# Performance work log

Measured on AMD Instinct MI355X. Metric: run time of the kernel, lower is better.

## Reference

```python
import jax, jax.numpy as jnp
import numpy as np

N = 100000      # nodes
E = 1600000     # edges (avg degree 16)
IN, HID, OUT = 128, 128, 64


def setup_inputs() -> dict:
    key = jax.random.key(0)
    k1, k2, k3, k4 = jax.random.split(key, 4)
    x = jax.random.normal(k1, (N, IN), dtype=jnp.float32)
    edge_index = jax.random.randint(k2, (2, E), 0, N, dtype=jnp.int64)
    # GCNConv linear weights (glorot-ish scale) and zero biases
    W1 = jax.random.normal(k3, (IN, HID), dtype=jnp.float32) * (1.0 / np.sqrt(IN))
    b1 = jnp.zeros((HID,), jnp.float32)
    W2 = jax.random.normal(k4, (HID, OUT), dtype=jnp.float32) * (1.0 / np.sqrt(HID))
    b2 = jnp.zeros((OUT,), jnp.float32)
    return {"x": x, "edge_index": edge_index, "W1": W1, "b1": b1, "W2": W2, "b2": b2}


def reference(x, edge_index, W1, b1, W2, b2):
    n = x.shape[0]
    loops = jnp.arange(n, dtype=edge_index.dtype)
    self_e = jnp.stack([loops, loops])  # [2, N]
    # forward() explicitly adds self-loops, then PyG GCNConv's gcn_norm
    # (add_self_loops=True by default) adds a second set -> duplicate (i,i) edges.
    ei = jnp.concatenate([edge_index, self_e, self_e], axis=1)
    row, col = ei[0], ei[1]  # source, target

    # symmetric normalization: deg over target index, norm_e = d^-1/2[row]*d^-1/2[col]
    deg = jax.ops.segment_sum(jnp.ones(row.shape, x.dtype), col, num_segments=n)
    dis = jax.lax.rsqrt(deg)  # deg >= 2 thanks to self-loops
    norm = dis[row] * dis[col]  # [E']

    def gcn_conv(h, W, b):
        h = h @ W                               # transform first (PyG order)
        msg = h[row] * norm[:, None]            # gather + per-edge scale
        agg = jax.ops.segment_sum(msg, col, num_segments=n)  # scatter-add
        return agg + b

    h = jax.nn.relu(gcn_conv(x, W1, b1))
    return gcn_conv(h, W2, b2)
```

## Files before the change

kernel.cpp:

```cpp
#include <hip/hip_runtime.h>
#include <hip/hip_fp16.h>

#define NPB   512
#define NBMAX 256
#define CHUNK 2048

using f16x4 = __attribute__((ext_vector_type(4))) _Float16;
using f32x4 = __attribute__((ext_vector_type(4))) float;

__device__ __forceinline__ int edge_at(const void* ei, int is64, long long pos) {
  return is64 ? (int)((const long long*)ei)[pos] : ((const int*)ei)[pos];
}

__global__ __launch_bounds__(256) void k_fillB(const void* __restrict__ ei,
                                               int E, int cap,
                                               int* __restrict__ bcur,
                                               int* __restrict__ tmp, int nb) {
  __shared__ int cntL[NBMAX], gofs[NBMAX], curL[NBMAX];
  __shared__ int sflag;
  int t = threadIdx.x;
  if (t == 0) sflag = 1;
  __syncthreads();
  if (t < 64 && ((const int*)ei)[2 * t + 1] != 0) sflag = 0;
  cntL[t] = 0;
  __syncthreads();
  int is64 = sflag;
  long long base = (long long)blockIdx.x * CHUNK;
  if (base >= E) return;
  int m = (int)min((long long)CHUNK, (long long)E - base);
  int val[8];
  int bkt[8];
#pragma unroll
  for (int i = 0; i < 8; ++i) {
    int idx = t + i * 256;
    if (idx < m) {
      int r = edge_at(ei, is64, base + idx);
      int c = edge_at(ei, is64, (long long)E + base + idx);
      int b = c >> 9;
      val[i] = ((c & 511) << 17) | r;
      bkt[i] = b;
      atomicAdd(&cntL[b], 1);
    }
  }
  __syncthreads();
  if (t < nb) {
    int c = cntL[t];
    gofs[t] = (c ? atomicAdd(&bcur[t], c) : 0) + t * cap;
    curL[t] = 0;
  }
  __syncthreads();
#pragma unroll
  for (int i = 0; i < 8; ++i) {
    if (t + i * 256 < m) {
      int b = bkt[i];
      int p = atomicAdd(&curL[b], 1);
      tmp[gofs[b] + p] = val[i];
    }
  }
}

__global__ __launch_bounds__(512) void k_fillC(const int* __restrict__ tmp,
                                               const int* __restrict__ bcur,
                                               int cap, int* __restrict__ rowptr,
                                               float* __restrict__ dis,
                                               int* __restrict__ esrc,
                                               int N, int nb) {
  __shared__ int cnt[NPB];
  __shared__ int loc[NPB];
  __shared__ int sh[NPB];
  __shared__ int bb[NBMAX];
  int b = blockIdx.x, t = threadIdx.x;
  int count = bcur[b];
  int beg = b * cap;
  int end = beg + count;
  int base_node = b << 9;
  if (t < NBMAX) bb[t] = (t < nb) ? bcur[t] : 0;
  cnt[t] = 0;
  __syncthreads();
  for (int off = 1; off < NBMAX; off <<= 1) {
    int x = 0;
    if (t >= off && t < NBMAX) x = bb[t - off];
    __syncthreads();
    if (t >= off && t < NBMAX) bb[t] += x;
    __syncthreads();
  }
  int outb = b ? bb[b - 1] : 0;
  if (b == 0 && t == 0) rowptr[N] = bb[nb - 1];
  for (int e = beg + t; e < end; e += 512)
    atomicAdd(&cnt[tmp[e] >> 17], 1);
  __syncthreads();
  int c0 = cnt[t];
  sh[t] = c0;
  __syncthreads();
  for (int off = 1; off < NPB; off <<= 1) {
    int x = 0;
    if (t >= off) x = sh[t - off];
    __syncthreads();
    if (t >= off) sh[t] += x;
    __syncthreads();
  }
  int pre = t ? sh[t - 1] : 0;
  loc[t] = outb + pre;
  int v = base_node + t;
  if (v < N) {
    rowptr[v] = outb + pre;
    dis[v] = rsqrtf((float)(c0 + 2));
  }
  __syncthreads();
  for (int e = beg + t; e < end; e += 512) {
    int u = tmp[e];
    int pos = atomicAdd(&loc[u >> 17], 1);
    esrc[pos] = u & 0x1FFFF;
  }
}

template <int BN, bool AHALF, bool PRESCALE>
__global__ __launch_bounds__(BN * 4) void k_gemm(const void* __restrict__ Av,
                                                 const float* __restrict__ W,
                                                 const float* __restrict__ dis,
                                                 __half* __restrict__ C,
                                                 int M, int tiles) {
  constexpr int THREADS = BN * 4;
  constexpr int CH = BN / 4;
  __shared__ _Float16 At[64][136];
  __shared__ float disL[64];
  int t = threadIdx.x;
  int lane = t & 63, w = t >> 6;
  int lrow = lane & 15;
  int kq = (lane >> 4) * 4;
  int col = w * 16 + lrow;

  f16x4 bfrag[8];
#pragma unroll
  for (int k8 = 0; k8 < 8; ++k8) {
    int kb = k8 * 16 + kq;
    bfrag[k8] = f16x4{(_Float16)W[(size_t)(kb + 0) * BN + col],
                      (_Float16)W[(size_t)(kb + 1) * BN + col],
                      (_Float16)W[(size_t)(kb + 2) * BN + col],
                      (_Float16)W[(size_t)(kb + 3) * BN + col]};
  }

  for (int tile = blockIdx.x; tile < tiles; tile += gridDim.x) {
    int row0 = tile * 64;
    __syncthreads();
#pragma unroll
    for (int i = 0; i < (64 * 32) / THREADS; ++i) {
      int idx = t + i * THREADS;
      int r = idx >> 5, c = (idx & 31) * 4;
      int gr = row0 + r;
      f16x4 hv = {0, 0, 0, 0};
      if (gr < M) {
        if constexpr (AHALF) {
          hv = *(const f16x4*)&((const _Float16*)Av)[(size_t)gr * 128 + c];
        } else {
          float4 v = *(const float4*)&((const float*)Av)[(size_t)gr * 128 + c];
          hv = f16x4{(_Float16)v.x, (_Float16)v.y, (_Float16)v.z, (_Float16)v.w};
        }
      }
      *(f16x4*)&At[r][c] = hv;
    }
    if constexpr (PRESCALE) {
      if (t < 64) {
        int gr = row0 + t;
        disL[t] = (gr < M) ? dis[gr] : 0.f;
      }
    }
    __syncthreads();
    f32x4 acc[4];
#pragma unroll
    for (int mt = 0; mt < 4; ++mt) acc[mt] = f32x4{0.f, 0.f, 0.f, 0.f};
#pragma unroll
    for (int k8 = 0; k8 < 8; ++k8) {
      int kk = k8 * 16 + kq;
      f16x4 a[4];
#pragma unroll
      for (int mt = 0; mt < 4; ++mt)
        a[mt] = *(const f16x4*)&At[mt * 16 + lrow][kk];
#pragma unroll
      for (int mt = 0; mt < 4; ++mt)
        acc[mt] = __builtin_amdgcn_mfma_f32_16x16x16f16(a[mt], bfrag[k8],
                                                        acc[mt], 0, 0, 0);
    }
    __syncthreads();
#pragma unroll
    for (int mt = 0; mt < 4; ++mt) {
      int rr = mt * 16 + kq;
#pragma unroll
      for (int reg = 0; reg < 4; ++reg) {
        float val = acc[mt][reg];
        if constexpr (PRESCALE) val *= disL[rr + reg];
        At[rr + reg][col] = (_Float16)val;
      }
    }
    __syncthreads();
#pragma unroll
    for (int i = 0; i < (64 * CH) / THREADS; ++i) {
      int idx = t + i * THREADS;
      int r = idx / CH, c = (idx % CH) * 4;
      int gr = row0 + r;
      if (gr < M)
        *(f16x4*)&C[(size_t)gr * BN + c] = *(const f16x4*)&At[r][c];
    }
  }
}

#define ACC4(u)                                                         \
  { __half2 p;                                                          \
    p = *(__half2*)&(u).x; a0 += __low2float(p); a1 += __high2float(p); \
    p = *(__half2*)&(u).y; a2 += __low2float(p); a3 += __high2float(p); }

__global__ __launch_bounds__(256) void k_gather128(const __half* __restrict__ t,
    const float* __restrict__ bias, const int* __restrict__ rowptr,
    const int* __restrict__ esrc, const float* __restrict__ dis,
    __half* __restrict__ o, int n) {
  int gw = (int)((blockIdx.x * blockDim.x + threadIdx.x) >> 6);
  int lane = threadIdx.x & 63;
  int nw = (int)((gridDim.x * blockDim.x) >> 6);
  int half = lane >> 5;
  int f = (lane & 31) * 4;
  for (int v = gw; v < n; v += nw) {
    float a0 = 0.f, a1 = 0.f, a2 = 0.f, a3 = 0.f;
    int beg = rowptr[v], end = rowptr[v + 1];
    int e = beg + half;
    for (; e + 14 < end; e += 16) {
      int s0 = esrc[e],      s1 = esrc[e + 2],  s2 = esrc[e + 4],  s3 = esrc[e + 6];
      int s4 = esrc[e + 8],  s5 = esrc[e + 10], s6 = esrc[e + 12], s7 = esrc[e + 14];
      uint2 u0 = *(const uint2*)&t[(size_t)s0 * 128 + f];
      uint2 u1 = *(const uint2*)&t[(size_t)s1 * 128 + f];
      uint2 u2 = *(const uint2*)&t[(size_t)s2 * 128 + f];
      uint2 u3 = *(const uint2*)&t[(size_t)s3 * 128 + f];
      uint2 u4 = *(const uint2*)&t[(size_t)s4 * 128 + f];
      uint2 u5 = *(const uint2*)&t[(size_t)s5 * 128 + f];
      uint2 u6 = *(const uint2*)&t[(size_t)s6 * 128 + f];
      uint2 u7 = *(const uint2*)&t[(size_t)s7 * 128 + f];
      ACC4(u0) ACC4(u1) ACC4(u2) ACC4(u3)
      ACC4(u4) ACC4(u5) ACC4(u6) ACC4(u7)
    }
    for (; e + 6 < end; e += 8) {
      int s0 = esrc[e], s1 = esrc[e + 2], s2 = esrc[e + 4], s3 = esrc[e + 6];
      uint2 u0 = *(const uint2*)&t[(size_t)s0 * 128 + f];
      uint2 u1 = *(const uint2*)&t[(size_t)s1 * 128 + f];
      uint2 u2 = *(const uint2*)&t[(size_t)s2 * 128 + f];
      uint2 u3 = *(const uint2*)&t[(size_t)s3 * 128 + f];
      ACC4(u0) ACC4(u1) ACC4(u2) ACC4(u3)
    }
    for (; e < end; e += 2) {
      int s0 = esrc[e];
      uint2 u0 = *(const uint2*)&t[(size_t)s0 * 128 + f];
      ACC4(u0)
    }
    if (half == 0) {
      uint2 uv = *(const uint2*)&t[(size_t)v * 128 + f];
      __half2 p;
      p = *(__half2*)&uv.x; a0 = fmaf(2.f, __low2float(p), a0); a1 = fmaf(2.f, __high2float(p), a1);
      p = *(__half2*)&uv.y; a2 = fmaf(2.f, __low2float(p), a2); a3 = fmaf(2.f, __high2float(p), a3);
    }
    a0 += __shfl_xor(a0, 32); a1 += __shfl_xor(a1, 32);
    a2 += __shfl_xor(a2, 32); a3 += __shfl_xor(a3, 32);
    if (half == 0) {
      float dv = dis[v];
      a0 = fmaxf(fmaf(dv, a0, bias[f]),     0.f);
      a1 = fmaxf(fmaf(dv, a1, bias[f + 1]), 0.f);
      a2 = fmaxf(fmaf(dv, a2, bias[f + 2]), 0.f);
      a3 = fmaxf(fmaf(dv, a3, bias[f + 3]), 0.f);
      __half2 h0 = __floats2half2_rn(a0, a1), h1 = __floats2half2_rn(a2, a3);
      uint2 uu;
      uu.x = *(unsigned int*)&h0; uu.y = *(unsigned int*)&h1;
      *(uint2*)&o[(size_t)v * 128 + f] = uu;
    }
  }
}

__global__ __launch_bounds__(256) void k_gather64(const __half* __restrict__ t,
    const float* __restrict__ bias, const int* __restrict__ rowptr,
    const int* __restrict__ esrc, const float* __restrict__ dis,
    float* __restrict__ o, int n) {
  int gw = (int)((blockIdx.x * blockDim.x + threadIdx.x) >> 6);
  int lane = threadIdx.x & 63;
  int nw = (int)((gridDim.x * blockDim.x) >> 6);
  int sub = lane >> 4;
  int f = (lane & 15) * 4;
  for (int v = gw; v < n; v += nw) {
    float a0 = 0.f, a1 = 0.f, a2 = 0.f, a3 = 0.f;
    int beg = rowptr[v], end = rowptr[v + 1];
    int e = beg + sub;
    for (; e + 28 < end; e += 32) {
      int s0 = esrc[e],      s1 = esrc[e + 4],  s2 = esrc[e + 8],  s3 = esrc[e + 12];
      int s4 = esrc[e + 16], s5 = esrc[e + 20], s6 = esrc[e + 24], s7 = esrc[e + 28];
      uint2 u0 = *(const uint2*)&t[(size_t)s0 * 64 + f];
      uint2 u1 = *(const uint2*)&t[(size_t)s1 * 64 + f];
      uint2 u2 = *(const uint2*)&t[(size_t)s2 * 64 + f];
      uint2 u3 = *(const uint2*)&t[(size_t)s3 * 64 + f];
      uint2 u4 = *(const uint2*)&t[(size_t)s4 * 64 + f];
      uint2 u5 = *(const uint2*)&t[(size_t)s5 * 64 + f];
      uint2 u6 = *(const uint2*)&t[(size_t)s6 * 64 + f];
      uint2 u7 = *(const uint2*)&t[(size_t)s7 * 64 + f];
      ACC4(u0) ACC4(u1) ACC4(u2) ACC4(u3)
      ACC4(u4) ACC4(u5) ACC4(u6) ACC4(u7)
    }
    for (; e + 12 < end; e += 16) {
      int s0 = esrc[e], s1 = esrc[e + 4], s2 = esrc[e + 8], s3 = esrc[e + 12];
      uint2 u0 = *(const uint2*)&t[(size_t)s0 * 64 + f];
      uint2 u1 = *(const uint2*)&t[(size_t)s1 * 64 + f];
      uint2 u2 = *(const uint2*)&t[(size_t)s2 * 64 + f];
      uint2 u3 = *(const uint2*)&t[(size_t)s3 * 64 + f];
      ACC4(u0) ACC4(u1) ACC4(u2) ACC4(u3)
    }
    for (; e < end; e += 4) {
      int s0 = esrc[e];
      uint2 u0 = *(const uint2*)&t[(size_t)s0 * 64 + f];
      ACC4(u0)
    }
    if (sub == 0) {
      uint2 uv = *(const uint2*)&t[(size_t)v * 64 + f];
      __half2 p;
      p = *(__half2*)&uv.x; a0 = fmaf(2.f, __low2float(p), a0); a1 = fmaf(2.f, __high2float(p), a1);
      p = *(__half2*)&uv.y; a2 = fmaf(2.f, __low2float(p), a2); a3 = fmaf(2.f, __high2float(p), a3);
    }
    a0 += __shfl_xor(a0, 16); a0 += __shfl_xor(a0, 32);
    a1 += __shfl_xor(a1, 16); a1 += __shfl_xor(a1, 32);
    a2 += __shfl_xor(a2, 16); a2 += __shfl_xor(a2, 32);
    a3 += __shfl_xor(a3, 16); a3 += __shfl_xor(a3, 32);
    if (sub == 0) {
      float dv = dis[v];
      float4 r;
      r.x = fmaf(dv, a0, bias[f]);     r.y = fmaf(dv, a1, bias[f + 1]);
      r.z = fmaf(dv, a2, bias[f + 2]); r.w = fmaf(dv, a3, bias[f + 3]);
      *(float4*)&o[(size_t)v * 64 + f] = r;
    }
  }
}

extern "C" void kernel_launch(void* const* d_in, const int* in_sizes, int n_in,
                              void* d_out, int out_size, void* d_ws, size_t ws_size,
                              hipStream_t stream) {
  const float* x  = (const float*)d_in[0];
  const void*  ei = d_in[1];
  const float* W1 = (const float*)d_in[2];
  const float* b1 = (const float*)d_in[3];
  const float* W2 = (const float*)d_in[4];
  const float* b2 = (const float*)d_in[5];
  const int N = in_sizes[0] / 128;
  const int E = in_sizes[1] / 2;
  float* out = (float*)d_out;
  const int nb  = (N + NPB - 1) / NPB;
  const int cap = E / nb + 4096;

  size_t off = 0;
  auto alloc = [&](size_t bytes) -> void* {
    void* p = (char*)d_ws + off;
    off += (bytes + 255) & ~(size_t)255;
    return p;
  };
  int*    bcur   = (int*)alloc(NBMAX * 4);
  int*    rowptr = (int*)alloc(((size_t)N + 1) * 4);
  float*  dis    = (float*)alloc((size_t)N * 4);
  int*    tmp    = (int*)alloc(((size_t)nb * cap + 16384) * 4);
  int*    esrc   = (int*)alloc((size_t)E * 4);
  __half* t1     = (__half*)alloc((size_t)N * 128 * 2);
  __half* z1     = (__half*)alloc((size_t)N * 128 * 2);
  __half* t2     = t1;

  int tiles = (N + 63) / 64;
  int nchunks = (E + CHUNK - 1) / CHUNK;

  hipMemsetAsync(bcur, 0, NBMAX * 4, stream);
  k_fillB<<<nchunks, 256, 0, stream>>>(ei, E, cap, bcur, tmp, nb);
  k_fillC<<<nb, 512, 0, stream>>>(tmp, bcur, cap, rowptr, dis, esrc, N, nb);

  k_gemm<128, false, true><<<tiles, 512, 0, stream>>>(x, W1, dis, t1, N, tiles);
  k_gather128<<<2048, 256, 0, stream>>>(t1, b1, rowptr, esrc, dis, z1, N);
  k_gemm<64, true, true><<<tiles, 256, 0, stream>>>(z1, W2, dis, t2, N, tiles);
  k_gather64<<<2048, 256, 0, stream>>>(t2, b2, rowptr, esrc, dis, out, N);
}
```

Before: 199.1 us.

## Fuse layer-1 aggregation with layer-2 GEMM via per-wave MFMA

Replaces the separate layer-1 gather kernel and second GEMM with one kernel. Each wave aggregates 16 nodes into LDS, then multiplies them by W2 with fp16 MFMA and scales by the degree norm. This removes the round trip of the 128-wide intermediate through global memory and one launch. In exchange it uses a fixed one-group-per-wave grid instead of grid-stride, and reloads W2 from global per wave.

```diff
diff --git a/kernel.cpp b/kernel.cpp
--- a/kernel.cpp
+++ b/kernel.cpp
@@ -209,64 +209,96 @@
     p = *(__half2*)&(u).x; a0 += __low2float(p); a1 += __high2float(p); \
     p = *(__half2*)&(u).y; a2 += __low2float(p); a3 += __high2float(p); }
 
-__global__ __launch_bounds__(256) void k_gather128(const __half* __restrict__ t,
+__global__ __launch_bounds__(256) void k_gfuse(const __half* __restrict__ t,
     const float* __restrict__ bias, const int* __restrict__ rowptr,
     const int* __restrict__ esrc, const float* __restrict__ dis,
-    __half* __restrict__ o, int n) {
-  int gw = (int)((blockIdx.x * blockDim.x + threadIdx.x) >> 6);
+    const float* __restrict__ W2, __half* __restrict__ t2, int n) {
+  __shared__ _Float16 Z[4][16][132];
+  __shared__ float disS[4][16];
+  int w = threadIdx.x >> 6;
   int lane = threadIdx.x & 63;
-  int nw = (int)((gridDim.x * blockDim.x) >> 6);
+  int g = blockIdx.x * 4 + w;
+  int v0 = g * 16;
+  if (v0 >= n) return;
   int half = lane >> 5;
   int f = (lane & 31) * 4;
-  for (int v = gw; v < n; v += nw) {
+  int lrow = lane & 15;
+  int kq = (lane >> 4) * 4;
+  if (lane < 16) disS[w][lane] = (v0 + lane < n) ? dis[v0 + lane] : 0.f;
+  float bb0 = bias[f], bb1 = bias[f + 1], bb2 = bias[f + 2], bb3 = bias[f + 3];
+
+  for (int nb_ = 0; nb_ < 16; ++nb_) {
+    int v = v0 + nb_;
     float a0 = 0.f, a1 = 0.f, a2 = 0.f, a3 = 0.f;
-    int beg = rowptr[v], end = rowptr[v + 1];
-    int e = beg + half;
-    for (; e + 14 < end; e += 16) {
-      int s0 = esrc[e],      s1 = esrc[e + 2],  s2 = esrc[e + 4],  s3 = esrc[e + 6];
-      int s4 = esrc[e + 8],  s5 = esrc[e + 10], s6 = esrc[e + 12], s7 = esrc[e + 14];
-      uint2 u0 = *(const uint2*)&t[(size_t)s0 * 128 + f];
-      uint2 u1 = *(const uint2*)&t[(size_t)s1 * 128 + f];
-      uint2 u2 = *(const uint2*)&t[(size_t)s2 * 128 + f];
-      uint2 u3 = *(const uint2*)&t[(size_t)s3 * 128 + f];
-      uint2 u4 = *(const uint2*)&t[(size_t)s4 * 128 + f];
-      uint2 u5 = *(const uint2*)&t[(size_t)s5 * 128 + f];
-      uint2 u6 = *(const uint2*)&t[(size_t)s6 * 128 + f];
-      uint2 u7 = *(const uint2*)&t[(size_t)s7 * 128 + f];
-      ACC4(u0) ACC4(u1) ACC4(u2) ACC4(u3)
-      ACC4(u4) ACC4(u5) ACC4(u6) ACC4(u7)
-    }
-    for (; e + 6 < end; e += 8) {
-      int s0 = esrc[e], s1 = esrc[e + 2], s2 = esrc[e + 4], s3 = esrc[e + 6];
-      uint2 u0 = *(const uint2*)&t[(size_t)s0 * 128 + f];
-      uint2 u1 = *(const uint2*)&t[(size_t)s1 * 128 + f];
-      uint2 u2 = *(const uint2*)&t[(size_t)s2 * 128 + f];
-      uint2 u3 = *(const uint2*)&t[(size_t)s3 * 128 + f];
-      ACC4(u0) ACC4(u1) ACC4(u2) ACC4(u3)
-    }
-    for (; e < end; e += 2) {
-      int s0 = esrc[e];
-      uint2 u0 = *(const uint2*)&t[(size_t)s0 * 128 + f];
-      ACC4(u0)
-    }
-    if (half == 0) {
-      uint2 uv = *(const uint2*)&t[(size_t)v * 128 + f];
-      __half2 p;
-      p = *(__half2*)&uv.x; a0 = fmaf(2.f, __low2float(p), a0); a1 = fmaf(2.f, __high2float(p), a1);
-      p = *(__half2*)&uv.y; a2 = fmaf(2.f, __low2float(p), a2); a3 = fmaf(2.f, __high2float(p), a3);
+    if (v < n) {
+      int beg = rowptr[v], end = rowptr[v + 1];
+      int e = beg + half;
+      for (; e + 14 < end; e += 16) {
+        int s0 = esrc[e],      s1 = esrc[e + 2],  s2 = esrc[e + 4],  s3 = esrc[e + 6];
+        int s4 = esrc[e + 8],  s5 = esrc[e + 10], s6 = esrc[e + 12], s7 = esrc[e + 14];
+        uint2 u0 = *(const uint2*)&t[(size_t)s0 * 128 + f];
+        uint2 u1 = *(const uint2*)&t[(size_t)s1 * 128 + f];
+        uint2 u2 = *(const uint2*)&t[(size_t)s2 * 128 + f];
+        uint2 u3 = *(const uint2*)&t[(size_t)s3 * 128 + f];
+        uint2 u4 = *(const uint2*)&t[(size_t)s4 * 128 + f];
+        uint2 u5 = *(const uint2*)&t[(size_t)s5 * 128 + f];
+        uint2 u6 = *(const uint2*)&t[(size_t)s6 * 128 + f];
+        uint2 u7 = *(const uint2*)&t[(size_t)s7 * 128 + f];
+        ACC4(u0) ACC4(u1) ACC4(u2) ACC4(u3)
+        ACC4(u4) ACC4(u5) ACC4(u6) ACC4(u7)
+      }
+      for (; e + 6 < end; e += 8) {
+        int s0 = esrc[e], s1 = esrc[e + 2], s2 = esrc[e + 4], s3 = esrc[e + 6];
+        uint2 u0 = *(const uint2*)&t[(size_t)s0 * 128 + f];
+        uint2 u1 = *(const uint2*)&t[(size_t)s1 * 128 + f];
+        uint2 u2 = *(const uint2*)&t[(size_t)s2 * 128 + f];
+        uint2 u3 = *(const uint2*)&t[(size_t)s3 * 128 + f];
+        ACC4(u0) ACC4(u1) ACC4(u2) ACC4(u3)
+      }
+      for (; e < end; e += 2) {
+        int s0 = esrc[e];
+        uint2 u0 = *(const uint2*)&t[(size_t)s0 * 128 + f];
+        ACC4(u0)
+      }
+      if (half == 0) {
+        uint2 uv = *(const uint2*)&t[(size_t)v * 128 + f];
+        __half2 p;
+        p = *(__half2*)&uv.x; a0 = fmaf(2.f, __low2float(p), a0); a1 = fmaf(2.f, __high2float(p), a1);
+        p = *(__half2*)&uv.y; a2 = fmaf(2.f, __low2float(p), a2); a3 = fmaf(2.f, __high2float(p), a3);
+      }
     }
     a0 += __shfl_xor(a0, 32); a1 += __shfl_xor(a1, 32);
     a2 += __shfl_xor(a2, 32); a3 += __shfl_xor(a3, 32);
     if (half == 0) {
-      float dv = dis[v];
-      a0 = fmaxf(fmaf(dv, a0, bias[f]),     0.f);
-      a1 = fmaxf(fmaf(dv, a1, bias[f + 1]), 0.f);
-      a2 = fmaxf(fmaf(dv, a2, bias[f + 2]), 0.f);
-      a3 = fmaxf(fmaf(dv, a3, bias[f + 3]), 0.f);
-      __half2 h0 = __floats2half2_rn(a0, a1), h1 = __floats2half2_rn(a2, a3);
-      uint2 uu;
-      uu.x = *(unsigned int*)&h0; uu.y = *(unsigned int*)&h1;
-      *(uint2*)&o[(size_t)v * 128 + f] = uu;
+      float dv = disS[w][nb_];
+      a0 = fmaxf(fmaf(dv, a0, bb0), 0.f);
+      a1 = fmaxf(fmaf(dv, a1, bb1), 0.f);
+      a2 = fmaxf(fmaf(dv, a2, bb2), 0.f);
+      a3 = fmaxf(fmaf(dv, a3, bb3), 0.f);
+      *(f16x4*)&Z[w][nb_][f] = f16x4{(_Float16)a0, (_Float16)a1,
+                                     (_Float16)a2, (_Float16)a3};
+    }
+  }
+#pragma unroll
+  for (int nt = 0; nt < 4; ++nt) {
+    f32x4 acc = {0.f, 0.f, 0.f, 0.f};
+    int col = nt * 16 + lrow;
+#pragma unroll
+    for (int k8 = 0; k8 < 8; ++k8) {
+      int kb = k8 * 16 + kq;
+      f16x4 a = *(const f16x4*)&Z[w][lrow][kb];
+      f16x4 b = f16x4{(_Float16)W2[(size_t)(kb + 0) * 64 + col],
+                      (_Float16)W2[(size_t)(kb + 1) * 64 + col],
+                      (_Float16)W2[(size_t)(kb + 2) * 64 + col],
+                      (_Float16)W2[(size_t)(kb + 3) * 64 + col]};
+      acc = __builtin_amdgcn_mfma_f32_16x16x16f16(a, b, acc, 0, 0, 0);
+    }
+#pragma unroll
+    for (int reg = 0; reg < 4; ++reg) {
+      int rr = kq + reg;
+      int gv = v0 + rr;
+      if (gv < n)
+        t2[(size_t)gv * 64 + col] = (_Float16)(acc[reg] * disS[w][rr]);
     }
   }
 }
@@ -358,8 +390,7 @@
   int*    tmp    = (int*)alloc(((size_t)nb * cap + 16384) * 4);
   int*    esrc   = (int*)alloc((size_t)E * 4);
   __half* t1     = (__half*)alloc((size_t)N * 128 * 2);
-  __half* z1     = (__half*)alloc((size_t)N * 128 * 2);
-  __half* t2     = t1;
+  __half* t2     = (__half*)alloc((size_t)N * 64 * 2);
 
   int tiles = (N + 63) / 64;
   int nchunks = (E + CHUNK - 1) / CHUNK;
@@ -369,7 +400,6 @@
   k_fillC<<<nb, 512, 0, stream>>>(tmp, bcur, cap, rowptr, dis, esrc, N, nb);
 
   k_gemm<128, false, true><<<tiles, 512, 0, stream>>>(x, W1, dis, t1, N, tiles);
-  k_gather128<<<2048, 256, 0, stream>>>(t1, b1, rowptr, esrc, dis, z1, N);
-  k_gemm<64, true, true><<<tiles, 256, 0, stream>>>(z1, W2, dis, t2, N, tiles);
+  k_gfuse<<<(N + 63) / 64, 256, 0, stream>>>(t1, b1, rowptr, esrc, dis, W2, t2, N);
   k_gather64<<<2048, 256, 0, stream>>>(t2, b2, rowptr, esrc, dis, out, N);
 }
```

After: 229.9 us. 15.5% more time.
